# Performance work log

Hardware: AMD Instinct MI355X
Metric: run time of the kernel (lower is better)

## Reference

```python
import jax, jax.numpy as jnp
import numpy as np

N, E, D, C, H1 = 50000, 800000, 128, 8, 2


def setup_inputs() -> dict:
    key = jax.random.key(0)
    ks = jax.random.split(key, 14)
    s = lambda k, sh: (jax.random.normal(k, sh, jnp.float32) * 0.05)
    return {
        "x": jax.random.normal(ks[0], (N, D), jnp.float32),
        "edge_index": jax.random.randint(ks[1], (2, E), 0, N, dtype=jnp.int32),
        # conv1: GATConv(D, D, heads=2, concat=True)
        "W1": s(ks[2], (D, H1 * D)),
        "att1_src": s(ks[3], (H1, D)),
        "att1_dst": s(ks[4], (H1, D)),
        "b1": s(ks[5], (H1 * D,)),
        # conv2: GATConv(2D, D, heads=1, concat=False)
        "W2": s(ks[6], (H1 * D, D)),
        "att2_src": s(ks[7], (1, D)),
        "att2_dst": s(ks[8], (1, D)),
        "b2": s(ks[9], (D,)),
        # MLP head
        "Wm1": s(ks[10], (D, D)),
        "bm1": s(ks[11], (D,)),
        "Wm2": s(ks[12], (D, C)),
        "bm2": s(ks[13], (C,)),
    }


def gat_conv(x, src, dst, W, a_src, a_dst, b, heads, out_ch, concat):
    """PyG GATConv (eval mode): self-loops added by caller, softmax over
    edges grouped by destination node, negative_slope=0.2."""
    n = x.shape[0]
    h = (x @ W).reshape(n, heads, out_ch)              # [N,H,F]
    alpha_src = jnp.einsum('nhf,hf->nh', h, a_src)     # [N,H]
    alpha_dst = jnp.einsum('nhf,hf->nh', h, a_dst)     # [N,H]
    e = jax.nn.leaky_relu(alpha_src[src] + alpha_dst[dst], 0.2)  # [E,H]
    e_max = jax.ops.segment_max(e, dst, num_segments=n)
    ex = jnp.exp(e - e_max[dst])
    denom = jax.ops.segment_sum(ex, dst, num_segments=n)
    alpha = ex / jnp.maximum(denom[dst], 1e-16)        # [E,H]
    out = jax.ops.segment_sum(h[src] * alpha[:, :, None], dst, num_segments=n)
    out = out.reshape(n, heads * out_ch) if concat else out.mean(axis=1)
    return out + b


def reference(x, edge_index, W1, att1_src, att1_dst, b1,
              W2, att2_src, att2_dst, b2, Wm1, bm1, Wm2, bm2):
    n = x.shape[0]
    loop = jnp.arange(n, dtype=edge_index.dtype)
    src = jnp.concatenate([edge_index[0], loop])  # add_self_loops=True
    dst = jnp.concatenate([edge_index[1], loop])
    h = jax.nn.elu(gat_conv(x, src, dst, W1, att1_src, att1_dst, b1, H1, D, True))
    h = jax.nn.elu(gat_conv(h, src, dst, W2, att2_src, att2_dst, b2, 1, D, False))
    h = jax.nn.relu(h @ Wm1 + bm1)
    return jax.nn.relu(h @ Wm2 + bm2)
```

## Files before the change

kernel.cpp:

```cpp
#include <hip/hip_runtime.h>
#include <hip/hip_bf16.h>


__device__ __forceinline__ float lrelu(float x){ return x > 0.f ? x : 0.2f*x; }
__device__ __forceinline__ float elu_f(float x){ return x > 0.f ? x : __expf(x) - 1.f; }
__device__ __forceinline__ unsigned short f2bf(float f){
  __hip_bfloat16 h = __float2bfloat16(f);
  return *reinterpret_cast<unsigned short*>(&h);
}
__device__ __forceinline__ float bflo(unsigned int u){ return __uint_as_float(u << 16); }
__device__ __forceinline__ float bfhi(unsigned int u){ return __uint_as_float(u & 0xffff0000u); }
__device__ __forceinline__ unsigned int packbf(float a, float b){
  return (unsigned int)f2bf(a) | ((unsigned int)f2bf(b) << 16);
}

typedef __attribute__((ext_vector_type(8))) short bf16x8;
typedef __attribute__((ext_vector_type(4))) float f32x4;

__global__ __launch_bounds__(256) void f2bf_fuse_kernel(
    const float* __restrict__ x, unsigned short* __restrict__ xb, int N,
    const float* __restrict__ va, float* __restrict__ as1, float* __restrict__ ad1,
    int* __restrict__ bcount, int* __restrict__ gcur, int NB)
{
  int i = blockIdx.x*256 + threadIdx.x;
  int total = N*32;
  float4 v = make_float4(0.f,0.f,0.f,0.f);
  if (i < total){
    v = ((const float4*)x)[i];
    ushort4 u; u.x=f2bf(v.x); u.y=f2bf(v.y); u.z=f2bf(v.z); u.w=f2bf(v.w);
    ((ushort4*)xb)[i] = u;
  }
  int c = (i & 31) << 2;
  float4 vs0 = *(const float4*)(va + c);
  float4 vs1 = *(const float4*)(va + 128 + c);
  float4 vd0 = *(const float4*)(va + 256 + c);
  float4 vd1 = *(const float4*)(va + 384 + c);
  float s0 = v.x*vs0.x + v.y*vs0.y + v.z*vs0.z + v.w*vs0.w;
  float s1 = v.x*vs1.x + v.y*vs1.y + v.z*vs1.z + v.w*vs1.w;
  float d0 = v.x*vd0.x + v.y*vd0.y + v.z*vd0.z + v.w*vd0.w;
  float d1 = v.x*vd1.x + v.y*vd1.y + v.z*vd1.z + v.w*vd1.w;
  #pragma unroll
  for (int m = 1; m <= 16; m <<= 1){
    s0 += __shfl_xor(s0, m); s1 += __shfl_xor(s1, m);
    d0 += __shfl_xor(d0, m); d1 += __shfl_xor(d1, m);
  }
  if ((i & 31) == 0 && i < total){
    int n = i >> 5;
    *(float2*)(as1 + 2*n) = make_float2(s0, s1);
    *(float2*)(ad1 + 2*n) = make_float2(d0, d1);
  }
  if (i < NB){ bcount[i] = 0; gcur[i] = 0; }
}

__global__ void va_kernel(const float* __restrict__ W1, const float* __restrict__ a1s,
                          const float* __restrict__ a1d, float* __restrict__ va){
  int idx = blockIdx.x*256 + threadIdx.x;
  if (idx >= 512) return;
  int v = idx >> 7, k = idx & 127;
  const float* avec = (v < 2) ? a1s : a1d;
  int head = v & 1;
  const float* wrow = W1 + (size_t)k*256 + head*128;
  const float* arow = avec + head*128;
  float s = 0.f;
  #pragma unroll 8
  for (int f = 0; f < 128; ++f) s += wrow[f]*arow[f];
  va[idx] = s;
}

__global__ __launch_bounds__(1024) void bhist_kernel(const int* __restrict__ dst, int E,
                                                     int* __restrict__ bcount, int NB){
  __shared__ int h[1024];
  for (int i = threadIdx.x; i < NB; i += 1024) h[i] = 0;
  __syncthreads();
  for (int e = blockIdx.x*1024 + threadIdx.x; e < E; e += gridDim.x*1024)
    atomicAdd(&h[dst[e] >> 6], 1);
  __syncthreads();
  for (int i = threadIdx.x; i < NB; i += 1024)
    if (h[i]) atomicAdd(&bcount[i], h[i]);
}

__global__ __launch_bounds__(1024) void bscan_kernel(const int* __restrict__ bcount,
                                                     int* __restrict__ boff, int NB){
  __shared__ int s[1024];
  int t = threadIdx.x;
  int mine = (t < NB) ? bcount[t] : 0;
  s[t] = mine;
  __syncthreads();
  for (int d = 1; d < 1024; d <<= 1){
    int v = (t >= d) ? s[t-d] : 0;
    __syncthreads();
    s[t] += v;
    __syncthreads();
  }
  if (t < NB) boff[t] = s[t] - mine;
  if (t == NB-1) boff[NB] = s[t];
}

__global__ __launch_bounds__(256) void bscatter_kernel(
    const int* __restrict__ src, const int* __restrict__ dst, int E,
    const int* __restrict__ boff, int* __restrict__ gcur,
    unsigned int* __restrict__ pairs, int NB)
{
  __shared__ int h[1024];
  __shared__ int runbase[1024];
  const int t = threadIdx.x;
  const int e0 = blockIdx.x * 4096;
  for (int i = t; i < NB; i += 256) h[i] = 0;
  __syncthreads();
  int myb[16]; unsigned int myw[16];
  #pragma unroll
  for (int q = 0; q < 16; ++q){
    int e = e0 + q*256 + t;
    int b = -1; unsigned int w = 0;
    if (e < E){
      int d = dst[e];
      b = d >> 6;
      w = ((unsigned int)(d & 63) << 26) | (unsigned int)src[e];
      atomicAdd(&h[b], 1);
    }
    myb[q] = b; myw[q] = w;
  }
  __syncthreads();
  for (int i = t; i < NB; i += 256)
    runbase[i] = h[i] ? atomicAdd(&gcur[i], h[i]) : 0;
  __syncthreads();
  for (int i = t; i < NB; i += 256) h[i] = 0;
  __syncthreads();
  #pragma unroll
  for (int q = 0; q < 16; ++q){
    if (myb[q] >= 0){
      int off = atomicAdd(&h[myb[q]], 1);
      pairs[(size_t)boff[myb[q]] + runbase[myb[q]] + off] = myw[q];
    }
  }
}

__global__ __launch_bounds__(256) void bbuild_kernel(
    const unsigned int* __restrict__ pairs, const int* __restrict__ boff,
    int* __restrict__ rowptr, int* __restrict__ csr, int N)
{
  __shared__ int deg[64], offs[64], cur[64];
  const int b = blockIdx.x;
  const int t = threadIdx.x;
  const int n0 = b << 6;
  const int nNodes = min(64, N - n0);
  const int p0 = boff[b], p1 = boff[b+1];
  const int base = p0 + n0;
  if (t < 64) deg[t] = (t < nNodes) ? 1 : 0;
  __syncthreads();
  for (int i = p0 + t; i < p1; i += 256)
    atomicAdd(&deg[pairs[i] >> 26], 1);
  __syncthreads();
  if (t < 64){
    int x = deg[t];
    #pragma unroll
    for (int d = 1; d < 64; d <<= 1){
      int y = __shfl_up(x, d);
      if (t >= d) x += y;
    }
    offs[t] = x - deg[t];
    cur[t] = 1;
    if (t < nNodes){
      rowptr[n0 + t + 1] = base + x;
      csr[base + x - deg[t]] = n0 + t;
    }
    if (b == 0 && t == 0) rowptr[0] = 0;
  }
  __syncthreads();
  for (int i = p0 + t; i < p1; i += 256){
    unsigned int w = pairs[i];
    int dl = w >> 26;
    int s  = (int)(w & 0x03ffffffu);
    int off = atomicAdd(&cur[dl], 1);
    csr[base + offs[dl] + off] = s;
  }
}

__global__ void wtrans_all_kernel(const float* __restrict__ W1, unsigned short* __restrict__ BT1a,
                                  unsigned short* __restrict__ BT1b,
                                  const float* __restrict__ W2, unsigned short* __restrict__ BT2,
                                  const float* __restrict__ Wm1, unsigned short* __restrict__ BT3){
  int idx = blockIdx.x*256 + threadIdx.x;
  const int S1 = 128*128, S2 = 128*256, S3 = 128*128;
  if (idx < S1){
    int n = idx >> 7, k = idx & 127;
    BT1a[idx] = f2bf(W1[(size_t)k*256 + n]);
    BT1b[idx] = f2bf(W1[(size_t)k*256 + 128 + n]);
  } else if (idx < S1 + S2){
    int j = idx - S1;
    int n = j >> 8, k = j & 255;
    BT2[j] = f2bf(W2[(size_t)k*128 + n]);
  } else if (idx < S1 + S2 + S3){
    int j = idx - S1 - S2;
    int n = j >> 7, k = j & 127;
    BT3[j] = f2bf(Wm1[(size_t)k*128 + n]);
  }
}

__global__ __launch_bounds__(256) void gemm_mfma_kernel(
    const unsigned short* __restrict__ A, int lda,
    const unsigned short* __restrict__ BT,
    void* __restrict__ Cv, int ldc, int M, int K,
    const float* __restrict__ bias, int act, int out_bf16)
{
  __shared__ unsigned short a_s[128*72];
  __shared__ unsigned short b_s[128*72];
  const int tid  = threadIdx.x;
  const int lane = tid & 63, wv = tid >> 6;
  const int r0 = blockIdx.y*128;
  const int mh = (wv & 1)*64, nh = (wv >> 1)*64;
  const int l15 = lane & 15, quad = lane >> 4;

  f32x4 acc[4][4];
  #pragma unroll
  for (int i = 0; i < 4; ++i)
    #pragma unroll
    for (int j = 0; j < 4; ++j)
      #pragma unroll
      for (int r = 0; r < 4; ++r) acc[i][j][r] = 0.f;

  const int srow = tid >> 3;
  const int skc  = tid & 7;

  for (int k0 = 0; k0 < K; k0 += 64){
    #pragma unroll
    for (int it = 0; it < 4; ++it){
      int row = it*32 + srow;
      int grow = r0 + row;
      uint4 v = make_uint4(0u,0u,0u,0u);
      if (grow < M) v = *(const uint4*)(A + (size_t)grow*lda + k0 + skc*8);
      *(uint4*)(&a_s[row*72 + skc*8]) = v;
    }
    #pragma unroll
    for (int it = 0; it < 4; ++it){
      int row = it*32 + srow;
      uint4 v = *(const uint4*)(BT + (size_t)row*K + k0 + skc*8);
      *(uint4*)(&b_s[row*72 + skc*8]) = v;
    }
    __syncthreads();
    #pragma unroll
    for (int ks = 0; ks < 64; ks += 32){
      bf16x8 af[4], bfr[4];
      #pragma unroll
      for (int i = 0; i < 4; ++i)
        af[i] = *(const bf16x8*)(&a_s[(mh + i*16 + l15)*72 + ks + quad*8]);
      #pragma unroll
      for (int j = 0; j < 4; ++j)
        bfr[j] = *(const bf16x8*)(&b_s[(nh + j*16 + l15)*72 + ks + quad*8]);
      #pragma unroll
      for (int i = 0; i < 4; ++i)
        #pragma unroll
        for (int j = 0; j < 4; ++j)
          acc[i][j] = __builtin_amdgcn_mfma_f32_16x16x32_bf16(bfr[j], af[i], acc[i][j], 0, 0, 0);
    }
    __syncthreads();
  }

  #pragma unroll
  for (int i = 0; i < 4; ++i){
    int m = r0 + mh + i*16 + l15;
    if (m < M){
      #pragma unroll
      for (int j = 0; j < 4; ++j){
        int n = nh + j*16 + quad*4;
        float4 bb = make_float4(0.f,0.f,0.f,0.f);
        if (bias) bb = *(const float4*)(bias + n);
        float o[4];
        #pragma unroll
        for (int r = 0; r < 4; ++r){
          float v = acc[i][j][r] + ((const float*)&bb)[r];
          if (act == 1) v = fmaxf(v, 0.f);
          else if (act == 2) v = elu_f(v);
          o[r] = v;
        }
        if (out_bf16){
          ushort4 u; u.x=f2bf(o[0]); u.y=f2bf(o[1]); u.z=f2bf(o[2]); u.w=f2bf(o[3]);
          *(ushort4*)((unsigned short*)Cv + (size_t)m*ldc + n) = u;
        } else {
          *(float4*)((float*)Cv + (size_t)m*ldc + n) = make_float4(o[0],o[1],o[2],o[3]);
        }
      }
    }
  }
}

__global__ __launch_bounds__(256) void asad2_kernel(
    const unsigned short* __restrict__ h2b, const float* __restrict__ att_src,
    const float* __restrict__ att_dst, float* __restrict__ as_, float* __restrict__ ad_, int N)
{
  int w = threadIdx.x >> 6, lane = threadIdx.x & 63;
  int n = blockIdx.x*4 + w;
  if (n >= N) return;
  int c = lane << 1;
  unsigned int u = *(const unsigned int*)(h2b + (size_t)n*128 + c);
  float2 ws2 = *(const float2*)(att_src + c);
  float2 wd2 = *(const float2*)(att_dst + c);
  float vx = bflo(u), vy = bfhi(u);
  float ps = vx*ws2.x + vy*ws2.y;
  float pd = vx*wd2.x + vy*wd2.y;
  #pragma unroll
  for (int m = 1; m <= 32; m <<= 1){ ps += __shfl_xor(ps, m); pd += __shfl_xor(pd, m); }
  if (lane == 0){ as_[n] = ps; ad_[n] = pd; }
}

__global__ __launch_bounds__(256) void agg1x_kernel(
    const unsigned short* __restrict__ xb, const float* __restrict__ as_,
    const float* __restrict__ ad_, const int* __restrict__ rowptr, const int* __restrict__ csr,
    unsigned short* __restrict__ xa, int N)
{
  const int wv = threadIdx.x >> 6, lane = threadIdx.x & 63;
  const int ql = lane & 15;
  const int n = blockIdx.x*16 + wv*4 + (lane >> 4);
  const bool valid = n < N;
  int start = 0, end = 0;
  float2 adv = make_float2(0.f, 0.f);
  if (valid){ start = rowptr[n]; end = rowptr[n+1]; adv = *(const float2*)(ad_ + 2*n); }

  int jl = start + ql;
  bool have = valid && (jl < end);
  int s_l = 0;
  float p0 = 0.f, p1 = 0.f;
  if (have){
    s_l = csr[jl];
    float2 av = *(const float2*)(as_ + 2*s_l);
    p0 = __expf(lrelu(av.x + adv.x));
    p1 = __expf(lrelu(av.y + adv.y));
  }
  float l0 = p0, l1 = p1;
  for (int j = jl + 16; j < end; j += 16){
    int s = csr[j];
    float2 av = *(const float2*)(as_ + 2*s);
    l0 += __expf(lrelu(av.x + adv.x));
    l1 += __expf(lrelu(av.y + adv.y));
  }
  #pragma unroll
  for (int msk = 1; msk <= 8; msk <<= 1){
    l0 += __shfl_xor(l0, msk);
    l1 += __shfl_xor(l1, msk);
  }
  float inv0 = 1.f / fmaxf(l0, 1e-16f);
  float inv1 = 1.f / fmaxf(l1, 1e-16f);
  float a0_l = p0 * inv0;
  float a1_l = p1 * inv1;

  float acc0[8], acc1[8];
  #pragma unroll
  for (int i = 0; i < 8; ++i){ acc0[i] = 0.f; acc1[i] = 0.f; }
  const int c = ql << 3;
  const unsigned short* hp = xb + c;

  int cnt = valid ? min(16, end - start) : 0;
  for (int t = 0; t < cnt; ++t){
    int   sA  = __shfl(s_l, t, 16);
    float a0A = __shfl(a0_l, t, 16);
    float a1A = __shfl(a1_l, t, 16);
    uint4 u = *(const uint4*)(hp + (sA << 7));
    float f0 = bflo(u.x), f1 = bfhi(u.x), f2v = bflo(u.y), f3 = bfhi(u.y);
    float f4 = bflo(u.z), f5 = bfhi(u.z), f6 = bflo(u.w), f7 = bfhi(u.w);
    acc0[0] += a0A*f0; acc0[1] += a0A*f1; acc0[2] += a0A*f2v; acc0[3] += a0A*f3;
    acc0[4] += a0A*f4; acc0[5] += a0A*f5; acc0[6] += a0A*f6;  acc0[7] += a0A*f7;
    acc1[0] += a1A*f0; acc1[1] += a1A*f1; acc1[2] += a1A*f2v; acc1[3] += a1A*f3;
    acc1[4] += a1A*f4; acc1[5] += a1A*f5; acc1[6] += a1A*f6;  acc1[7] += a1A*f7;
  }
  for (int jb = start + 16; jb < end; jb += 16){
    int jl2 = jb + ql;
    int s2 = 0; float a0_2 = 0.f, a1_2 = 0.f;
    if (jl2 < end){
      s2 = csr[jl2];
      float2 av = *(const float2*)(as_ + 2*s2);
      a0_2 = __expf(lrelu(av.x + adv.x)) * inv0;
      a1_2 = __expf(lrelu(av.y + adv.y)) * inv1;
    }
    int cnt2 = min(16, end - jb);
    for (int t2 = 0; t2 < cnt2; ++t2){
      int   sA  = __shfl(s2, t2, 16);
      float a0A = __shfl(a0_2, t2, 16);
      float a1A = __shfl(a1_2, t2, 16);
      uint4 u = *(const uint4*)(hp + (sA << 7));
      float f0 = bflo(u.x), f1 = bfhi(u.x), f2v = bflo(u.y), f3 = bfhi(u.y);
      float f4 = bflo(u.z), f5 = bfhi(u.z), f6 = bflo(u.w), f7 = bfhi(u.w);
      acc0[0] += a0A*f0; acc0[1] += a0A*f1; acc0[2] += a0A*f2v; acc0[3] += a0A*f3;
      acc0[4] += a0A*f4; acc0[5] += a0A*f5; acc0[6] += a0A*f6;  acc0[7] += a0A*f7;
      acc1[0] += a1A*f0; acc1[1] += a1A*f1; acc1[2] += a1A*f2v; acc1[3] += a1A*f3;
      acc1[4] += a1A*f4; acc1[5] += a1A*f5; acc1[6] += a1A*f6;  acc1[7] += a1A*f7;
    }
  }

  if (valid){
    uint4 u0, u1;
    u0.x = packbf(acc0[0], acc0[1]); u0.y = packbf(acc0[2], acc0[3]);
    u0.z = packbf(acc0[4], acc0[5]); u0.w = packbf(acc0[6], acc0[7]);
    u1.x = packbf(acc1[0], acc1[1]); u1.y = packbf(acc1[2], acc1[3]);
    u1.z = packbf(acc1[4], acc1[5]); u1.w = packbf(acc1[6], acc1[7]);
    *(uint4*)(xa + (size_t)n*256 + c)       = u0;
    *(uint4*)(xa + (size_t)n*256 + 128 + c) = u1;
  }
}

__global__ __launch_bounds__(256) void agg2_kernel(
    const unsigned short* __restrict__ h2b, const float* __restrict__ as_,
    const float* __restrict__ ad_, const int* __restrict__ rowptr, const int* __restrict__ csr,
    const float* __restrict__ b2, unsigned short* __restrict__ outb, int N)
{
  const int wv = threadIdx.x >> 6, lane = threadIdx.x & 63;
  const int ql = lane & 15;
  const int n = blockIdx.x*16 + wv*4 + (lane >> 4);
  const bool valid = n < N;
  int start = 0, end = 0;
  float adn = 0.f;
  if (valid){ start = rowptr[n]; end = rowptr[n+1]; adn = ad_[n]; }

  int jl = start + ql;
  bool have = valid && (jl < end);
  int s_l = 0;
  float p_l = 0.f;
  if (have){
    s_l = csr[jl];
    p_l = __expf(lrelu(as_[s_l] + adn));
  }
  float l = p_l;
  for (int j = jl + 16; j < end; j += 16)
    l += __expf(lrelu(as_[csr[j]] + adn));
  #pragma unroll
  for (int msk = 1; msk <= 8; msk <<= 1) l += __shfl_xor(l, msk);
  float inv = 1.f / fmaxf(l, 1e-16f);
  float a_l = p_l * inv;

  float acc[8];
  #pragma unroll
  for (int i = 0; i < 8; ++i) acc[i] = 0.f;
  const int c = ql << 3;
  const unsigned short* hp = h2b + c;

  int cnt = valid ? min(16, end - start) : 0;
  int t = 0;
  for (; t + 1 < cnt; t += 2){
    int   sA = __shfl(s_l, t, 16),  sB = __shfl(s_l, t+1, 16);
    float aA = __shfl(a_l, t, 16),  aB = __shfl(a_l, t+1, 16);
    uint4 uA = *(const uint4*)(hp + (sA << 7));
    uint4 uB = *(const uint4*)(hp + (sB << 7));
    acc[0] += aA*bflo(uA.x) + aB*bflo(uB.x);
    acc[1] += aA*bfhi(uA.x) + aB*bfhi(uB.x);
    acc[2] += aA*bflo(uA.y) + aB*bflo(uB.y);
    acc[3] += aA*bfhi(uA.y) + aB*bfhi(uB.y);
    acc[4] += aA*bflo(uA.z) + aB*bflo(uB.z);
    acc[5] += aA*bfhi(uA.z) + aB*bfhi(uB.z);
    acc[6] += aA*bflo(uA.w) + aB*bflo(uB.w);
    acc[7] += aA*bfhi(uA.w) + aB*bfhi(uB.w);
  }
  if (t < cnt){
    int   sA = __shfl(s_l, t, 16);
    float aA = __shfl(a_l, t, 16);
    uint4 uA = *(const uint4*)(hp + (sA << 7));
    acc[0] += aA*bflo(uA.x); acc[1] += aA*bfhi(uA.x);
    acc[2] += aA*bflo(uA.y); acc[3] += aA*bfhi(uA.y);
    acc[4] += aA*bflo(uA.z); acc[5] += aA*bfhi(uA.z);
    acc[6] += aA*bflo(uA.w); acc[7] += aA*bfhi(uA.w);
  }
  for (int jb = start + 16; jb < end; jb += 16){
    int jl2 = jb + ql;
    int s2 = 0; float a2 = 0.f;
    if (jl2 < end){
      s2 = csr[jl2];
      a2 = __expf(lrelu(as_[s2] + adn)) * inv;
    }
    int cnt2 = min(16, end - jb);
    for (int t2 = 0; t2 < cnt2; ++t2){
      int   sA = __shfl(s2, t2, 16);
      float aA = __shfl(a2, t2, 16);
      uint4 uA = *(const uint4*)(hp + (sA << 7));
      acc[0] += aA*bflo(uA.x); acc[1] += aA*bfhi(uA.x);
      acc[2] += aA*bflo(uA.y); acc[3] += aA*bfhi(uA.y);
      acc[4] += aA*bflo(uA.z); acc[5] += aA*bfhi(uA.z);
      acc[6] += aA*bflo(uA.w); acc[7] += aA*bfhi(uA.w);
    }
  }

  if (valid){
    float4 bb0 = *(const float4*)(b2 + c);
    float4 bb1 = *(const float4*)(b2 + c + 4);
    float o[8];
    o[0]=elu_f(acc[0]+bb0.x); o[1]=elu_f(acc[1]+bb0.y);
    o[2]=elu_f(acc[2]+bb0.z); o[3]=elu_f(acc[3]+bb0.w);
    o[4]=elu_f(acc[4]+bb1.x); o[5]=elu_f(acc[5]+bb1.y);
    o[6]=elu_f(acc[6]+bb1.z); o[7]=elu_f(acc[7]+bb1.w);
    uint4 up;
    up.x = packbf(o[0], o[1]); up.y = packbf(o[2], o[3]);
    up.z = packbf(o[4], o[5]); up.w = packbf(o[6], o[7]);
    *(uint4*)(outb + (size_t)n*128 + c) = up;
  }
}

__global__ __launch_bounds__(256) void mlp2_kernel(
    const float* __restrict__ hid, const float* __restrict__ Wm2,
    const float* __restrict__ bm2, float* __restrict__ out, int N)
{
  int w = threadIdx.x >> 6, lane = threadIdx.x & 63;
  int n = blockIdx.x*4 + w;
  if (n >= N) return;
  int o = lane & 7, kg = lane >> 3;
  float p = 0.f;
  #pragma unroll
  for (int i = 0; i < 16; ++i){
    int k = kg*16 + i;
    p += hid[(size_t)n*128 + k] * Wm2[k*8 + o];
  }
  p += __shfl_xor(p, 8);
  p += __shfl_xor(p, 16);
  p += __shfl_xor(p, 32);
  if (kg == 0) out[(size_t)n*8 + o] = fmaxf(p + bm2[o], 0.f);
}

extern "C" void kernel_launch(void* const* d_in, const int* in_sizes, int n_in,
                              void* d_out, int out_size, void* d_ws, size_t ws_size,
                              hipStream_t stream)
{
  (void)n_in; (void)out_size; (void)ws_size;
  const float* x   = (const float*)d_in[0];
  const int*   ei  = (const int*)d_in[1];
  const float* W1  = (const float*)d_in[2];
  const float* a1s = (const float*)d_in[3];
  const float* a1d = (const float*)d_in[4];
  const float* b1  = (const float*)d_in[5];
  const float* W2  = (const float*)d_in[6];
  const float* a2s = (const float*)d_in[7];
  const float* a2d = (const float*)d_in[8];
  const float* b2  = (const float*)d_in[9];
  const float* Wm1 = (const float*)d_in[10];
  const float* bm1 = (const float*)d_in[11];
  const float* Wm2 = (const float*)d_in[12];
  const float* bm2 = (const float*)d_in[13];
  float* out = (float*)d_out;

  const int N = in_sizes[0] / 128;
  const int E = in_sizes[1] / 2;
  const int NB = (N + 63) >> 6;
  const int* srcp = ei;
  const int* dstp = ei + E;

  char* ws = (char*)d_ws;
  unsigned short* xb    = (unsigned short*)ws;
  unsigned short* xa    = (unsigned short*)(ws + (size_t)N*256);
  unsigned short* out1b = (unsigned short*)(ws + (size_t)N*768);
  unsigned short* h2b   = (unsigned short*)(ws + (size_t)N*1280);
  char* tail = ws + (size_t)N*1536;
  unsigned short* BT1a = (unsigned short*)tail;
  unsigned short* BT1b = BT1a + 128*128;
  unsigned short* BT2  = BT1b + 128*128;
  unsigned short* BT3  = BT2 + 128*256;
  float* va   = (float*)(BT3 + 128*128);
  float* as1  = va + 512;
  float* ad1  = as1 + (size_t)2*N;
  float* as2  = ad1 + (size_t)2*N;
  float* ad2  = as2 + N;
  int* bcount = (int*)(ad2 + N);
  int* boff   = bcount + 1024;
  int* gcur   = boff + 1032;
  int* rowptr = gcur + 1024;
  int* csr    = rowptr + N + 1;
  unsigned int* pairs = (unsigned int*)(csr + E + N);

  unsigned short* gb = xb;
  float* hid = (float*)xa;

  va_kernel<<<2, 256, 0, stream>>>(W1, a1s, a1d, va);
  f2bf_fuse_kernel<<<(N*32 + 255)/256, 256, 0, stream>>>(x, xb, N, va, as1, ad1,
                                                         bcount, gcur, NB);
  bhist_kernel<<<64, 1024, 0, stream>>>(dstp, E, bcount, NB);
  bscan_kernel<<<1, 1024, 0, stream>>>(bcount, boff, NB);
  bscatter_kernel<<<(E + 4095)/4096, 256, 0, stream>>>(srcp, dstp, E, boff, gcur, pairs, NB);
  bbuild_kernel<<<NB, 256, 0, stream>>>(pairs, boff, rowptr, csr, N);
  wtrans_all_kernel<<<(128*128 + 128*256 + 128*128 + 255)/256, 256, 0, stream>>>(
      W1, BT1a, BT1b, W2, BT2, Wm1, BT3);

  const int gy   = (N + 127) / 128;
  const int nb4  = (N + 3) / 4;
  const int nb16 = (N + 15) / 16;

  agg1x_kernel<<<nb16, 256, 0, stream>>>(xb, as1, ad1, rowptr, csr, xa, N);
  gemm_mfma_kernel<<<dim3(1, gy), 256, 0, stream>>>(xa,       256, BT1a, out1b,       256, N, 128, b1,       2, 1);
  gemm_mfma_kernel<<<dim3(1, gy), 256, 0, stream>>>(xa + 128, 256, BT1b, out1b + 128, 256, N, 128, b1 + 128, 2, 1);
  gemm_mfma_kernel<<<dim3(1, gy), 256, 0, stream>>>(out1b, 256, BT2, h2b, 128, N, 256, nullptr, 0, 1);
  asad2_kernel<<<nb4, 256, 0, stream>>>(h2b, a2s, a2d, as2, ad2, N);
  agg2_kernel<<<nb16, 256, 0, stream>>>(h2b, as2, ad2, rowptr, csr, b2, gb, N);
  gemm_mfma_kernel<<<dim3(1, gy), 256, 0, stream>>>(gb, 128, BT3, hid, 128, N, 128, bm1, 1, 0);
  mlp2_kernel<<<nb4, 256, 0, stream>>>(hid, Wm2, bm2, out, N);
}
```

Baseline: 300.5 us.

## Fuse prep, histogram, attention-score and MLP epilogues into fewer kernels

Merges the weight transposes, attention-vector precompute and counter zeroing into one prep kernel. The bf16 conversion shares a launch with the edge histogram, and the two conv1 GEMMs become one 2D grid. The conv2 attention scores are computed in the GEMM epilogue, and the final 128x8 MLP layer is folded into the MLP GEMM epilogue. This cuts several launches and removes the fp32 hidden-tensor round trip and the separate asad2 pass, at the cost of heavier epilogues and more register and shared-memory use. The conv2 scores now come from fp32 accumulators rather than bf16-rounded values.

New measurement: 267.4 us. 11.0% less time.

```diff
diff --git a/kernel.cpp b/kernel.cpp
--- a/kernel.cpp
+++ b/kernel.cpp
@@ -17,169 +17,13 @@
 typedef __attribute__((ext_vector_type(8))) short bf16x8;
 typedef __attribute__((ext_vector_type(4))) float f32x4;
 
-__global__ __launch_bounds__(256) void f2bf_fuse_kernel(
-    const float* __restrict__ x, unsigned short* __restrict__ xb, int N,
-    const float* __restrict__ va, float* __restrict__ as1, float* __restrict__ ad1,
-    int* __restrict__ bcount, int* __restrict__ gcur, int NB)
-{
-  int i = blockIdx.x*256 + threadIdx.x;
-  int total = N*32;
-  float4 v = make_float4(0.f,0.f,0.f,0.f);
-  if (i < total){
-    v = ((const float4*)x)[i];
-    ushort4 u; u.x=f2bf(v.x); u.y=f2bf(v.y); u.z=f2bf(v.z); u.w=f2bf(v.w);
-    ((ushort4*)xb)[i] = u;
-  }
-  int c = (i & 31) << 2;
-  float4 vs0 = *(const float4*)(va + c);
-  float4 vs1 = *(const float4*)(va + 128 + c);
-  float4 vd0 = *(const float4*)(va + 256 + c);
-  float4 vd1 = *(const float4*)(va + 384 + c);
-  float s0 = v.x*vs0.x + v.y*vs0.y + v.z*vs0.z + v.w*vs0.w;
-  float s1 = v.x*vs1.x + v.y*vs1.y + v.z*vs1.z + v.w*vs1.w;
-  float d0 = v.x*vd0.x + v.y*vd0.y + v.z*vd0.z + v.w*vd0.w;
-  float d1 = v.x*vd1.x + v.y*vd1.y + v.z*vd1.z + v.w*vd1.w;
-  #pragma unroll
-  for (int m = 1; m <= 16; m <<= 1){
-    s0 += __shfl_xor(s0, m); s1 += __shfl_xor(s1, m);
-    d0 += __shfl_xor(d0, m); d1 += __shfl_xor(d1, m);
-  }
-  if ((i & 31) == 0 && i < total){
-    int n = i >> 5;
-    *(float2*)(as1 + 2*n) = make_float2(s0, s1);
-    *(float2*)(ad1 + 2*n) = make_float2(d0, d1);
-  }
-  if (i < NB){ bcount[i] = 0; gcur[i] = 0; }
-}
-
-__global__ void va_kernel(const float* __restrict__ W1, const float* __restrict__ a1s,
-                          const float* __restrict__ a1d, float* __restrict__ va){
-  int idx = blockIdx.x*256 + threadIdx.x;
-  if (idx >= 512) return;
-  int v = idx >> 7, k = idx & 127;
-  const float* avec = (v < 2) ? a1s : a1d;
-  int head = v & 1;
-  const float* wrow = W1 + (size_t)k*256 + head*128;
-  const float* arow = avec + head*128;
-  float s = 0.f;
-  #pragma unroll 8
-  for (int f = 0; f < 128; ++f) s += wrow[f]*arow[f];
-  va[idx] = s;
-}
-
-__global__ __launch_bounds__(1024) void bhist_kernel(const int* __restrict__ dst, int E,
-                                                     int* __restrict__ bcount, int NB){
-  __shared__ int h[1024];
-  for (int i = threadIdx.x; i < NB; i += 1024) h[i] = 0;
-  __syncthreads();
-  for (int e = blockIdx.x*1024 + threadIdx.x; e < E; e += gridDim.x*1024)
-    atomicAdd(&h[dst[e] >> 6], 1);
-  __syncthreads();
-  for (int i = threadIdx.x; i < NB; i += 1024)
-    if (h[i]) atomicAdd(&bcount[i], h[i]);
-}
-
-__global__ __launch_bounds__(1024) void bscan_kernel(const int* __restrict__ bcount,
-                                                     int* __restrict__ boff, int NB){
-  __shared__ int s[1024];
-  int t = threadIdx.x;
-  int mine = (t < NB) ? bcount[t] : 0;
-  s[t] = mine;
-  __syncthreads();
-  for (int d = 1; d < 1024; d <<= 1){
-    int v = (t >= d) ? s[t-d] : 0;
-    __syncthreads();
-    s[t] += v;
-    __syncthreads();
-  }
-  if (t < NB) boff[t] = s[t] - mine;
-  if (t == NB-1) boff[NB] = s[t];
-}
-
-__global__ __launch_bounds__(256) void bscatter_kernel(
-    const int* __restrict__ src, const int* __restrict__ dst, int E,
-    const int* __restrict__ boff, int* __restrict__ gcur,
-    unsigned int* __restrict__ pairs, int NB)
-{
-  __shared__ int h[1024];
-  __shared__ int runbase[1024];
-  const int t = threadIdx.x;
-  const int e0 = blockIdx.x * 4096;
-  for (int i = t; i < NB; i += 256) h[i] = 0;
-  __syncthreads();
-  int myb[16]; unsigned int myw[16];
-  #pragma unroll
-  for (int q = 0; q < 16; ++q){
-    int e = e0 + q*256 + t;
-    int b = -1; unsigned int w = 0;
-    if (e < E){
-      int d = dst[e];
-      b = d >> 6;
-      w = ((unsigned int)(d & 63) << 26) | (unsigned int)src[e];
-      atomicAdd(&h[b], 1);
-    }
-    myb[q] = b; myw[q] = w;
-  }
-  __syncthreads();
-  for (int i = t; i < NB; i += 256)
-    runbase[i] = h[i] ? atomicAdd(&gcur[i], h[i]) : 0;
-  __syncthreads();
-  for (int i = t; i < NB; i += 256) h[i] = 0;
-  __syncthreads();
-  #pragma unroll
-  for (int q = 0; q < 16; ++q){
-    if (myb[q] >= 0){
-      int off = atomicAdd(&h[myb[q]], 1);
-      pairs[(size_t)boff[myb[q]] + runbase[myb[q]] + off] = myw[q];
-    }
-  }
-}
-
-__global__ __launch_bounds__(256) void bbuild_kernel(
-    const unsigned int* __restrict__ pairs, const int* __restrict__ boff,
-    int* __restrict__ rowptr, int* __restrict__ csr, int N)
-{
-  __shared__ int deg[64], offs[64], cur[64];
-  const int b = blockIdx.x;
-  const int t = threadIdx.x;
-  const int n0 = b << 6;
-  const int nNodes = min(64, N - n0);
-  const int p0 = boff[b], p1 = boff[b+1];
-  const int base = p0 + n0;
-  if (t < 64) deg[t] = (t < nNodes) ? 1 : 0;
-  __syncthreads();
-  for (int i = p0 + t; i < p1; i += 256)
-    atomicAdd(&deg[pairs[i] >> 26], 1);
-  __syncthreads();
-  if (t < 64){
-    int x = deg[t];
-    #pragma unroll
-    for (int d = 1; d < 64; d <<= 1){
-      int y = __shfl_up(x, d);
-      if (t >= d) x += y;
-    }
-    offs[t] = x - deg[t];
-    cur[t] = 1;
-    if (t < nNodes){
-      rowptr[n0 + t + 1] = base + x;
-      csr[base + x - deg[t]] = n0 + t;
-    }
-    if (b == 0 && t == 0) rowptr[0] = 0;
-  }
-  __syncthreads();
-  for (int i = p0 + t; i < p1; i += 256){
-    unsigned int w = pairs[i];
-    int dl = w >> 26;
-    int s  = (int)(w & 0x03ffffffu);
-    int off = atomicAdd(&cur[dl], 1);
-    csr[base + offs[dl] + off] = s;
-  }
-}
-
-__global__ void wtrans_all_kernel(const float* __restrict__ W1, unsigned short* __restrict__ BT1a,
-                                  unsigned short* __restrict__ BT1b,
-                                  const float* __restrict__ W2, unsigned short* __restrict__ BT2,
-                                  const float* __restrict__ Wm1, unsigned short* __restrict__ BT3){
+__global__ void prep_kernel(const float* __restrict__ W1, unsigned short* __restrict__ BT1a,
+                            unsigned short* __restrict__ BT1b,
+                            const float* __restrict__ W2, unsigned short* __restrict__ BT2,
+                            const float* __restrict__ Wm1, unsigned short* __restrict__ BT3,
+                            const float* __restrict__ a1s, const float* __restrict__ a1d,
+                            float* __restrict__ va, int* __restrict__ bcount,
+                            int* __restrict__ gcur, int NB){
   int idx = blockIdx.x*256 + threadIdx.x;
   const int S1 = 128*128, S2 = 128*256, S3 = 128*128;
   if (idx < S1){
@@ -194,33 +38,184 @@
     int j = idx - S1 - S2;
     int n = j >> 7, k = j & 127;
     BT3[j] = f2bf(Wm1[(size_t)k*128 + n]);
-  }
-}
-
-__global__ __launch_bounds__(256) void gemm_mfma_kernel(
+  } else if (idx < S1 + S2 + S3 + 512){
+    int j = idx - S1 - S2 - S3;
+    int v = j >> 7, k = j & 127;
+    const float* avec = (v < 2) ? a1s : a1d;
+    int head = v & 1;
+    const float* wrow = W1 + (size_t)k*256 + head*128;
+    const float* arow = avec + head*128;
+    float s = 0.f;
+    #pragma unroll 8
+    for (int f = 0; f < 128; ++f) s += wrow[f]*arow[f];
+    va[j] = s;
+  } else if (idx < S1 + S2 + S3 + 512 + 2048){
+    int z = idx - (S1 + S2 + S3 + 512);
+    if (z < 1024){ if (z < NB) bcount[z] = 0; }
+    else { z -= 1024; if (z < NB) gcur[z] = 0; }
+  }
+}
+
+__global__ __launch_bounds__(256) void f2bf_hist_kernel(
+    const float* __restrict__ x, unsigned short* __restrict__ xb, int N,
+    const float* __restrict__ va, float* __restrict__ as1, float* __restrict__ ad1,
+    const int* __restrict__ dst, int E, int* __restrict__ bcount, int NB, int nbConv)
+{
+  __shared__ int h[1024];
+  if ((int)blockIdx.x < nbConv){
+    int i = blockIdx.x*256 + threadIdx.x;
+    int total = N*32;
+    float4 v = make_float4(0.f,0.f,0.f,0.f);
+    if (i < total){
+      v = ((const float4*)x)[i];
+      ushort4 u; u.x=f2bf(v.x); u.y=f2bf(v.y); u.z=f2bf(v.z); u.w=f2bf(v.w);
+      ((ushort4*)xb)[i] = u;
+    }
+    int c = (i & 31) << 2;
+    float4 vs0 = *(const float4*)(va + c);
+    float4 vs1 = *(const float4*)(va + 128 + c);
+    float4 vd0 = *(const float4*)(va + 256 + c);
+    float4 vd1 = *(const float4*)(va + 384 + c);
+    float s0 = v.x*vs0.x + v.y*vs0.y + v.z*vs0.z + v.w*vs0.w;
+    float s1 = v.x*vs1.x + v.y*vs1.y + v.z*vs1.z + v.w*vs1.w;
+    float d0 = v.x*vd0.x + v.y*vd0.y + v.z*vd0.z + v.w*vd0.w;
+    float d1 = v.x*vd1.x + v.y*vd1.y + v.z*vd1.z + v.w*vd1.w;
+    #pragma unroll
+    for (int m = 1; m <= 16; m <<= 1){
+      s0 += __shfl_xor(s0, m); s1 += __shfl_xor(s1, m);
+      d0 += __shfl_xor(d0, m); d1 += __shfl_xor(d1, m);
+    }
+    if ((i & 31) == 0 && i < total){
+      int n = i >> 5;
+      *(float2*)(as1 + 2*n) = make_float2(s0, s1);
+      *(float2*)(ad1 + 2*n) = make_float2(d0, d1);
+    }
+  } else {
+    for (int i = threadIdx.x; i < NB; i += 256) h[i] = 0;
+    __syncthreads();
+    int b0 = blockIdx.x - nbConv;
+    for (int e = b0*256 + threadIdx.x; e < E; e += 64*256)
+      atomicAdd(&h[dst[e] >> 6], 1);
+    __syncthreads();
+    for (int i = threadIdx.x; i < NB; i += 256)
+      if (h[i]) atomicAdd(&bcount[i], h[i]);
+  }
+}
+
+__global__ __launch_bounds__(1024) void bscan_kernel(const int* __restrict__ bcount,
+                                                     int* __restrict__ boff, int NB){
+  __shared__ int s[1024];
+  int t = threadIdx.x;
+  int mine = (t < NB) ? bcount[t] : 0;
+  s[t] = mine;
+  __syncthreads();
+  for (int d = 1; d < 1024; d <<= 1){
+    int v = (t >= d) ? s[t-d] : 0;
+    __syncthreads();
+    s[t] += v;
+    __syncthreads();
+  }
+  if (t < NB) boff[t] = s[t] - mine;
+  if (t == NB-1) boff[NB] = s[t];
+}
+
+__global__ __launch_bounds__(256) void bscatter_kernel(
+    const int* __restrict__ src, const int* __restrict__ dst, int E,
+    const int* __restrict__ boff, int* __restrict__ gcur,
+    unsigned int* __restrict__ pairs, int NB)
+{
+  __shared__ int h[1024];
+  __shared__ int runbase[1024];
+  const int t = threadIdx.x;
+  const int e0 = blockIdx.x * 4096;
+  for (int i = t; i < NB; i += 256) h[i] = 0;
+  __syncthreads();
+  int myb[16]; unsigned int myw[16];
+  #pragma unroll
+  for (int q = 0; q < 16; ++q){
+    int e = e0 + q*256 + t;
+    int b = -1; unsigned int w = 0;
+    if (e < E){
+      int d = dst[e];
+      b = d >> 6;
+      w = ((unsigned int)(d & 63) << 26) | (unsigned int)src[e];
+      atomicAdd(&h[b], 1);
+    }
+    myb[q] = b; myw[q] = w;
+  }
+  __syncthreads();
+  for (int i = t; i < NB; i += 256)
+    runbase[i] = h[i] ? atomicAdd(&gcur[i], h[i]) : 0;
+  __syncthreads();
+  for (int i = t; i < NB; i += 256) h[i] = 0;
+  __syncthreads();
+  #pragma unroll
+  for (int q = 0; q < 16; ++q){
+    if (myb[q] >= 0){
+      int off = atomicAdd(&h[myb[q]], 1);
+      pairs[(size_t)boff[myb[q]] + runbase[myb[q]] + off] = myw[q];
+    }
+  }
+}
+
+__global__ __launch_bounds__(256) void bbuild_kernel(
+    const unsigned int* __restrict__ pairs, const int* __restrict__ boff,
+    int* __restrict__ rowptr, int* __restrict__ csr, int N)
+{
+  __shared__ int deg[64], offs[64], cur[64];
+  const int b = blockIdx.x;
+  const int t = threadIdx.x;
+  const int n0 = b << 6;
+  const int nNodes = min(64, N - n0);
+  const int p0 = boff[b], p1 = boff[b+1];
+  const int base = p0 + n0;
+  if (t < 64) deg[t] = (t < nNodes) ? 1 : 0;
+  __syncthreads();
+  for (int i = p0 + t; i < p1; i += 256)
+    atomicAdd(&deg[pairs[i] >> 26], 1);
+  __syncthreads();
+  if (t < 64){
+    int x = deg[t];
+    #pragma unroll
+    for (int d = 1; d < 64; d <<= 1){
+      int y = __shfl_up(x, d);
+      if (t >= d) x += y;
+    }
+    offs[t] = x - deg[t];
+    cur[t] = 1;
+    if (t < nNodes){
+      rowptr[n0 + t + 1] = base + x;
+      csr[base + x - deg[t]] = n0 + t;
+    }
+    if (b == 0 && t == 0) rowptr[0] = 0;
+  }
+  __syncthreads();
+  for (int i = p0 + t; i < p1; i += 256){
+    unsigned int w = pairs[i];
+    int dl = w >> 26;
+    int s  = (int)(w & 0x03ffffffu);
+    int off = atomicAdd(&cur[dl], 1);
+    csr[base + offs[dl] + off] = s;
+  }
+}
+
+__device__ __forceinline__ void gemm_core(
     const unsigned short* __restrict__ A, int lda,
-    const unsigned short* __restrict__ BT,
-    void* __restrict__ Cv, int ldc, int M, int K,
-    const float* __restrict__ bias, int act, int out_bf16)
-{
-  __shared__ unsigned short a_s[128*72];
-  __shared__ unsigned short b_s[128*72];
+    const unsigned short* __restrict__ BT, int M, int K, int r0,
+    unsigned short* a_s, unsigned short* b_s, f32x4 (&acc)[4][4])
+{
   const int tid  = threadIdx.x;
   const int lane = tid & 63, wv = tid >> 6;
-  const int r0 = blockIdx.y*128;
   const int mh = (wv & 1)*64, nh = (wv >> 1)*64;
   const int l15 = lane & 15, quad = lane >> 4;
-
-  f32x4 acc[4][4];
+  const int srow = tid >> 3, skc = tid & 7;
+
   #pragma unroll
   for (int i = 0; i < 4; ++i)
     #pragma unroll
     for (int j = 0; j < 4; ++j)
       #pragma unroll
       for (int r = 0; r < 4; ++r) acc[i][j][r] = 0.f;
-
-  const int srow = tid >> 3;
-  const int skc  = tid & 7;
 
   for (int k0 = 0; k0 < K; k0 += 64){
     #pragma unroll
@@ -255,7 +250,27 @@
     }
     __syncthreads();
   }
-
+}
+
+__global__ __launch_bounds__(256) void gemm_conv1_kernel(
+    const unsigned short* __restrict__ xa, const unsigned short* __restrict__ BT1a,
+    const unsigned short* __restrict__ BT1b, unsigned short* __restrict__ out1b,
+    int M, const float* __restrict__ b1)
+{
+  __shared__ unsigned short a_s[128*72];
+  __shared__ unsigned short b_s[128*72];
+  const int hx = blockIdx.x;
+  const unsigned short* A  = xa + hx*128;
+  const unsigned short* BT = hx ? BT1b : BT1a;
+  unsigned short* C = out1b + hx*128;
+  const float* bias = b1 + hx*128;
+  const int r0 = blockIdx.y*128;
+  f32x4 acc[4][4];
+  gemm_core(A, 256, BT, M, 128, r0, a_s, b_s, acc);
+
+  const int lane = threadIdx.x & 63, wv = threadIdx.x >> 6;
+  const int mh = (wv & 1)*64, nh = (wv >> 1)*64;
+  const int l15 = lane & 15, quad = lane >> 4;
   #pragma unroll
   for (int i = 0; i < 4; ++i){
     int m = r0 + mh + i*16 + l15;
@@ -263,44 +278,136 @@
       #pragma unroll
       for (int j = 0; j < 4; ++j){
         int n = nh + j*16 + quad*4;
-        float4 bb = make_float4(0.f,0.f,0.f,0.f);
-        if (bias) bb = *(const float4*)(bias + n);
-        float o[4];
+        float4 bb = *(const float4*)(bias + n);
+        ushort4 u;
+        u.x = f2bf(elu_f(acc[i][j][0] + bb.x));
+        u.y = f2bf(elu_f(acc[i][j][1] + bb.y));
+        u.z = f2bf(elu_f(acc[i][j][2] + bb.z));
+        u.w = f2bf(elu_f(acc[i][j][3] + bb.w));
+        *(ushort4*)(C + (size_t)m*256 + n) = u;
+      }
+    }
+  }
+}
+
+__global__ __launch_bounds__(256) void gemm_conv2_kernel(
+    const unsigned short* __restrict__ out1b, const unsigned short* __restrict__ BT2,
+    unsigned short* __restrict__ h2b, int M,
+    const float* __restrict__ a2s, const float* __restrict__ a2d,
+    float* __restrict__ as2, float* __restrict__ ad2)
+{
+  __shared__ unsigned short a_s[128*72];
+  __shared__ unsigned short b_s[128*72];
+  __shared__ float part_s[128][2];
+  __shared__ float part_d[128][2];
+  const int r0 = blockIdx.y*128;
+  f32x4 acc[4][4];
+  gemm_core(out1b, 256, BT2, M, 256, r0, a_s, b_s, acc);
+
+  const int tid = threadIdx.x;
+  const int lane = tid & 63, wv = tid >> 6;
+  const int mh = (wv & 1)*64, nh = (wv >> 1)*64;
+  const int l15 = lane & 15, quad = lane >> 4;
+  #pragma unroll
+  for (int i = 0; i < 4; ++i){
+    int m = r0 + mh + i*16 + l15;
+    float ps = 0.f, pd = 0.f;
+    #pragma unroll
+    for (int j = 0; j < 4; ++j){
+      int n = nh + j*16 + quad*4;
+      float4 wsv = *(const float4*)(a2s + n);
+      float4 wdv = *(const float4*)(a2d + n);
+      float v0 = acc[i][j][0], v1 = acc[i][j][1], v2 = acc[i][j][2], v3 = acc[i][j][3];
+      ps += v0*wsv.x + v1*wsv.y + v2*wsv.z + v3*wsv.w;
+      pd += v0*wdv.x + v1*wdv.y + v2*wdv.z + v3*wdv.w;
+      if (m < M){
+        ushort4 u;
+        u.x = f2bf(v0); u.y = f2bf(v1); u.z = f2bf(v2); u.w = f2bf(v3);
+        *(ushort4*)(h2b + (size_t)m*128 + n) = u;
+      }
+    }
+    ps += __shfl_xor(ps, 16); ps += __shfl_xor(ps, 32);
+    pd += __shfl_xor(pd, 16); pd += __shfl_xor(pd, 32);
+    if (quad == 0){
+      part_s[mh + i*16 + l15][wv >> 1] = ps;
+      part_d[mh + i*16 + l15][wv >> 1] = pd;
+    }
+  }
+  __syncthreads();
+  if (tid < 128){
+    int gm = r0 + tid;
+    if (gm < M){
+      as2[gm] = part_s[tid][0] + part_s[tid][1];
+      ad2[gm] = part_d[tid][0] + part_d[tid][1];
+    }
+  }
+}
+
+__global__ __launch_bounds__(256) void gemm_mlp_kernel(
+    const unsigned short* __restrict__ gb, const unsigned short* __restrict__ BT3,
+    int M, const float* __restrict__ bm1, const float* __restrict__ Wm2,
+    const float* __restrict__ bm2, float* __restrict__ out)
+{
+  __shared__ unsigned short a_s[128*72];
+  __shared__ unsigned short b_s[128*72];
+  __shared__ float wm2_s[128*8];
+  __shared__ float part[128][2][8];
+  const int tid = threadIdx.x;
+  {
+    int i4 = tid*4;
+    *(float4*)(&wm2_s[i4]) = *(const float4*)(Wm2 + i4);
+  }
+  const int r0 = blockIdx.y*128;
+  f32x4 acc[4][4];
+  gemm_core(gb, 128, BT3, M, 128, r0, a_s, b_s, acc);
+
+  const int lane = tid & 63, wv = tid >> 6;
+  const int mh = (wv & 1)*64, nh = (wv >> 1)*64;
+  const int l15 = lane & 15, quad = lane >> 4;
+  #pragma unroll
+  for (int i = 0; i < 4; ++i){
+    float po[8];
+    #pragma unroll
+    for (int o = 0; o < 8; ++o) po[o] = 0.f;
+    #pragma unroll
+    for (int j = 0; j < 4; ++j){
+      int n = nh + j*16 + quad*4;
+      float4 bb = *(const float4*)(bm1 + n);
+      #pragma unroll
+      for (int r = 0; r < 4; ++r){
+        float hcol = fmaxf(acc[i][j][r] + ((const float*)&bb)[r], 0.f);
+        const float* wr = &wm2_s[(n + r)*8];
         #pragma unroll
-        for (int r = 0; r < 4; ++r){
-          float v = acc[i][j][r] + ((const float*)&bb)[r];
-          if (act == 1) v = fmaxf(v, 0.f);
-          else if (act == 2) v = elu_f(v);
-          o[r] = v;
-        }
-        if (out_bf16){
-          ushort4 u; u.x=f2bf(o[0]); u.y=f2bf(o[1]); u.z=f2bf(o[2]); u.w=f2bf(o[3]);
-          *(ushort4*)((unsigned short*)Cv + (size_t)m*ldc + n) = u;
-        } else {
-          *(float4*)((float*)Cv + (size_t)m*ldc + n) = make_float4(o[0],o[1],o[2],o[3]);
-        }
+        for (int o = 0; o < 8; ++o) po[o] += hcol*wr[o];
       }
     }
-  }
-}
-
-__global__ __launch_bounds__(256) void asad2_kernel(
-    const unsigned short* __restrict__ h2b, const float* __restrict__ att_src,
-    const float* __restrict__ att_dst, float* __restrict__ as_, float* __restrict__ ad_, int N)
-{
-  int w = threadIdx.x >> 6, lane = threadIdx.x & 63;
-  int n = blockIdx.x*4 + w;
-  if (n >= N) return;
-  int c = lane << 1;
-  unsigned int u = *(const unsigned int*)(h2b + (size_t)n*128 + c);
-  float2 ws2 = *(const float2*)(att_src + c);
-  float2 wd2 = *(const float2*)(att_dst + c);
-  float vx = bflo(u), vy = bfhi(u);
-  float ps = vx*ws2.x + vy*ws2.y;
-  float pd = vx*wd2.x + vy*wd2.y;
-  #pragma unroll
-  for (int m = 1; m <= 32; m <<= 1){ ps += __shfl_xor(ps, m); pd += __shfl_xor(pd, m); }
-  if (lane == 0){ as_[n] = ps; ad_[n] = pd; }
+    #pragma unroll
+    for (int o = 0; o < 8; ++o){
+      po[o] += __shfl_xor(po[o], 16);
+      po[o] += __shfl_xor(po[o], 32);
+    }
+    if (quad == 0){
+      #pragma unroll
+      for (int o = 0; o < 8; ++o) part[mh + i*16 + l15][wv >> 1][o] = po[o];
+    }
+  }
+  __syncthreads();
+  if (tid < 128){
+    int gm = r0 + tid;
+    if (gm < M){
+      float4 o0, o1;
+      o0.x = fmaxf(part[tid][0][0] + part[tid][1][0] + bm2[0], 0.f);
+      o0.y = fmaxf(part[tid][0][1] + part[tid][1][1] + bm2[1], 0.f);
+      o0.z = fmaxf(part[tid][0][2] + part[tid][1][2] + bm2[2], 0.f);
+      o0.w = fmaxf(part[tid][0][3] + part[tid][1][3] + bm2[3], 0.f);
+      o1.x = fmaxf(part[tid][0][4] + part[tid][1][4] + bm2[4], 0.f);
+      o1.y = fmaxf(part[tid][0][5] + part[tid][1][5] + bm2[5], 0.f);
+      o1.z = fmaxf(part[tid][0][6] + part[tid][1][6] + bm2[6], 0.f);
+      o1.w = fmaxf(part[tid][0][7] + part[tid][1][7] + bm2[7], 0.f);
+      *(float4*)(out + (size_t)gm*8)     = o0;
+      *(float4*)(out + (size_t)gm*8 + 4) = o1;
+    }
+  }
 }
 
 __global__ __launch_bounds__(256) void agg1x_kernel(
@@ -489,26 +596,6 @@
     up.z = packbf(o[4], o[5]); up.w = packbf(o[6], o[7]);
     *(uint4*)(outb + (size_t)n*128 + c) = up;
   }
-}
-
-__global__ __launch_bounds__(256) void mlp2_kernel(
-    const float* __restrict__ hid, const float* __restrict__ Wm2,
-    const float* __restrict__ bm2, float* __restrict__ out, int N)
-{
-  int w = threadIdx.x >> 6, lane = threadIdx.x & 63;
-  int n = blockIdx.x*4 + w;
-  if (n >= N) return;
-  int o = lane & 7, kg = lane >> 3;
-  float p = 0.f;
-  #pragma unroll
-  for (int i = 0; i < 16; ++i){
-    int k = kg*16 + i;
-    p += hid[(size_t)n*128 + k] * Wm2[k*8 + o];
-  }
-  p += __shfl_xor(p, 8);
-  p += __shfl_xor(p, 16);
-  p += __shfl_xor(p, 32);
-  if (kg == 0) out[(size_t)n*8 + o] = fmaxf(p + bm2[o], 0.f);
 }
 
 extern "C" void kernel_launch(void* const* d_in, const int* in_sizes, int n_in,
@@ -561,28 +648,24 @@
   unsigned int* pairs = (unsigned int*)(csr + E + N);
 
   unsigned short* gb = xb;
-  float* hid = (float*)xa;
-
-  va_kernel<<<2, 256, 0, stream>>>(W1, a1s, a1d, va);
-  f2bf_fuse_kernel<<<(N*32 + 255)/256, 256, 0, stream>>>(x, xb, N, va, as1, ad1,
-                                                         bcount, gcur, NB);
-  bhist_kernel<<<64, 1024, 0, stream>>>(dstp, E, bcount, NB);
+
+  const int nbConv = (N*32 + 255)/256;
+  const int prepTotal = 128*128 + 128*256 + 128*128 + 512 + 2048;
+
+  prep_kernel<<<(prepTotal + 255)/256, 256, 0, stream>>>(
+      W1, BT1a, BT1b, W2, BT2, Wm1, BT3, a1s, a1d, va, bcount, gcur, NB);
+  f2bf_hist_kernel<<<nbConv + 64, 256, 0, stream>>>(x, xb, N, va, as1, ad1,
+                                                    dstp, E, bcount, NB, nbConv);
   bscan_kernel<<<1, 1024, 0, stream>>>(bcount, boff, NB);
   bscatter_kernel<<<(E + 4095)/4096, 256, 0, stream>>>(srcp, dstp, E, boff, gcur, pairs, NB);
   bbuild_kernel<<<NB, 256, 0, stream>>>(pairs, boff, rowptr, csr, N);
-  wtrans_all_kernel<<<(128*128 + 128*256 + 128*128 + 255)/256, 256, 0, stream>>>(
-      W1, BT1a, BT1b, W2, BT2, Wm1, BT3);
 
   const int gy   = (N + 127) / 128;
-  const int nb4  = (N + 3) / 4;
   const int nb16 = (N + 15) / 16;
 
   agg1x_kernel<<<nb16, 256, 0, stream>>>(xb, as1, ad1, rowptr, csr, xa, N);
-  gemm_mfma_kernel<<<dim3(1, gy), 256, 0, stream>>>(xa,       256, BT1a, out1b,       256, N, 128, b1,       2, 1);
-  gemm_mfma_kernel<<<dim3(1, gy), 256, 0, stream>>>(xa + 128, 256, BT1b, out1b + 128, 256, N, 128, b1 + 128, 2, 1);
-  gemm_mfma_kernel<<<dim3(1, gy), 256, 0, stream>>>(out1b, 256, BT2, h2b, 128, N, 256, nullptr, 0, 1);
-  asad2_kernel<<<nb4, 256, 0, stream>>>(h2b, a2s, a2d, as2, ad2, N);
+  gemm_conv1_kernel<<<dim3(2, gy), 256, 0, stream>>>(xa, BT1a, BT1b, out1b, N, b1);
+  gemm_conv2_kernel<<<dim3(1, gy), 256, 0, stream>>>(out1b, BT2, h2b, N, a2s, a2d, as2, ad2);
   agg2_kernel<<<nb16, 256, 0, stream>>>(h2b, as2, ad2, rowptr, csr, b2, gb, N);
-  gemm_mfma_kernel<<<dim3(1, gy), 256, 0, stream>>>(gb, 128, BT3, hid, 128, N, 128, bm1, 1, 0);
-  mlp2_kernel<<<nb4, 256, 0, stream>>>(hid, Wm2, bm2, out, N);
-}
+  gemm_mlp_kernel<<<dim3(1, gy), 256, 0, stream>>>(gb, BT3, N, bm1, Wm2, bm2, out);
+}
```
